# Kernel tuning notes

Measured on AMD Instinct MI355X. Metric: run time of the kernel, lower is better.

The kernel has to match this reference:

```python
import jax, jax.numpy as jnp
import numpy as np

B, C, H, W = 16, 256, 32, 32
N_HEAD, DIM_HEAD = 8, 32  # dim_hidden = 256 == C


def setup_inputs() -> dict:
    key = jax.random.key(0)
    ks = jax.random.split(key, 9)
    s = 1.0 / np.sqrt(C)
    return {
        "x": jax.random.normal(ks[0], (B, C, H, W), dtype=jnp.float32),
        "w_q": jax.random.normal(ks[1], (C, C), dtype=jnp.float32) * s,
        "b_q": jnp.zeros((C,), dtype=jnp.float32),
        "w_k": jax.random.normal(ks[2], (C, C), dtype=jnp.float32) * s,
        "b_k": jnp.zeros((C,), dtype=jnp.float32),
        "w_v": jax.random.normal(ks[3], (C, C), dtype=jnp.float32) * s,
        "b_v": jnp.zeros((C,), dtype=jnp.float32),
        "w_o": jax.random.normal(ks[4], (C, C), dtype=jnp.float32) * s,
        "b_o": jnp.zeros((C,), dtype=jnp.float32),
    }


def reference(x, w_q, b_q, w_k, b_k, w_v, b_v, w_o, b_o):
    b, c, h, w = x.shape
    L = h * w
    scale = DIM_HEAD ** (-0.5)
    xf = x.reshape(b, c, L)  # [b, c, L]

    def proj(wm, bm):
        # 1x1 conv == per-position linear over channels
        y = jnp.einsum('oc,bcl->bol', wm, xf) + bm[None, :, None]
        return y.reshape(b, N_HEAD, DIM_HEAD, L)

    q = proj(w_q, b_q) * scale
    k = proj(w_k, b_k)
    v = proj(w_v, b_v)

    sim = jnp.einsum('bndl,bndm->bnlm', q, k)           # [b, n, L, L]
    att = jax.nn.softmax(sim, axis=-1)
    out = jnp.einsum('bnlm,bndm->bndl', att, v)         # [b, n, d, L]
    out = out.reshape(b, c, L)
    out = jnp.einsum('oc,bcl->bol', w_o, out) + b_o[None, :, None]
    return out.reshape(b, c, h, w)
```

## Files before the change

kernel.cpp:

```cpp
#include <hip/hip_runtime.h>
#include <hip/hip_bf16.h>
#include <math.h>

namespace {
constexpr int B_ = 16, C_ = 256, L_ = 1024, NH_ = 8, DH_ = 32;

typedef __attribute__((ext_vector_type(8))) short short8v;
typedef __attribute__((ext_vector_type(4))) float float4v;

__device__ __forceinline__ short f2bf(float f) {
    unsigned u = __builtin_bit_cast(unsigned, f);
    u += 0x7fffu + ((u >> 16) & 1u);
    return (short)(u >> 16);
}
__device__ __forceinline__ float bf2f(short s) {
    unsigned u = ((unsigned)(unsigned short)s) << 16;
    return __builtin_bit_cast(float, u);
}
__device__ __forceinline__ unsigned pkrn(float a, float b) {
    float2 f; f.x = a; f.y = b;
    __hip_bfloat162 h = __float22bfloat162_rn(f);
    unsigned u;
    __builtin_memcpy(&u, &h, sizeof(u));
    return u;
}
__device__ __forceinline__ void gld16(const short* g, short* l) {
    __builtin_amdgcn_global_load_lds(
        (const __attribute__((address_space(1))) unsigned*)g,
        (__attribute__((address_space(3))) unsigned*)l, 16, 0, 0);
}

__global__ __launch_bounds__(256) void xpose_kernel(
    const float* __restrict__ x, short* __restrict__ xthi)
{
    const int lt = blockIdx.x, ct = blockIdx.y, b = blockIdx.z;
    const int t = threadIdx.x;
    __shared__ float sX[64][68];

#pragma unroll
    for (int e = 0; e < 4; ++e) {
        const int row = e * 16 + (t >> 4);
        const int col = (t & 15) * 4;
        float4 v = *(const float4*)&x[((size_t)b * C_ + ct * 64 + row) * L_ + lt * 64 + col];
        *(float4*)&sX[row][col] = v;
    }
    __syncthreads();

    const int l = t & 63, cg = t >> 6;
    short hi[16];
#pragma unroll
    for (int i = 0; i < 16; ++i) hi[i] = f2bf(sX[cg * 16 + i][l]);
    const size_t base = ((size_t)b * L_ + lt * 64 + l) * C_ + ct * 64 + cg * 16;
    *(short8v*)&xthi[base]     = *(short8v*)&hi[0];
    *(short8v*)&xthi[base + 8] = *(short8v*)&hi[8];
}

__global__ __launch_bounds__(256) void stackw_kernel(
    const float* __restrict__ wq, const float* __restrict__ wk,
    const float* __restrict__ wv, const float* __restrict__ wo,
    short* __restrict__ WA, short* __restrict__ WoA)
{
    const int g = blockIdx.x * 256 + threadIdx.x;
    if (g < 768 * 256) {
        const int o = g >> 8, cc = g & 255;
        const float* src = (o < 256) ? wq : (o < 512) ? wk : wv;
        const float v = src[(size_t)(o & 255) * 256 + cc];
        const short hi = f2bf(v);
        const short lo = f2bf(v - bf2f(hi));
        WA[(size_t)o * 512 + cc]       = hi;
        WA[(size_t)o * 512 + 256 + cc] = lo;
    } else {
        const int g2 = g - 768 * 256;
        const int o = g2 >> 8, cc = g2 & 255;
        const float v = wo[(size_t)o * 256 + cc];
        const short hi = f2bf(v);
        const short lo = f2bf(v - bf2f(hi));
        WoA[(size_t)o * 512 + cc]       = hi;
        WoA[(size_t)o * 512 + 256 + cc] = lo;
    }
}

template <int KTOT, int EPI>
__global__ __launch_bounds__(256, 2) void gemm_kernel(
    const short* __restrict__ A, const short* __restrict__ B0,
    const float* __restrict__ bias0, const float* __restrict__ bias1, const float* __restrict__ bias2,
    float qscale, void* __restrict__ out0, void* __restrict__ out1, void* __restrict__ out2)
{
    const int lt = blockIdx.x, ot = blockIdx.y, b = blockIdx.z;
    const int t = threadIdx.x, wv = t >> 6, lane = t & 63;
    const int quad = lane >> 4, c = lane & 15;
    const int wo = (wv & 1) * 64, wl = (wv >> 1) * 64;

    __shared__ short sA[128 * 32];
    __shared__ short sB[128 * 32];

    float4v acc[4][4];
#pragma unroll
    for (int i = 0; i < 4; ++i)
#pragma unroll
        for (int j = 0; j < 4; ++j) acc[i][j] = (float4v)0.f;

    const short* Arow = A + (size_t)(ot * 128) * KTOT;
    const int srow = t >> 2, sseg = t & 3;

    for (int kk = 0; kk < KTOT / 32; ++kk) {
        const int koff = (kk & 7) * 32;
        __syncthreads();
#pragma unroll
        for (int e = 0; e < 2; ++e) {
            gld16(Arow + (size_t)(e * 64 + srow) * KTOT + kk * 32 + sseg * 8,
                  &sA[(e * 256 + t) * 8]);
            gld16(B0 + ((size_t)b * L_ + lt * 128 + e * 64 + srow) * 256 + koff + sseg * 8,
                  &sB[(e * 256 + t) * 8]);
        }
        __syncthreads();

        short8v af[4], bf[4];
#pragma unroll
        for (int i = 0; i < 4; ++i) af[i] = *(const short8v*)&sA[(wo + 16 * i + c) * 32 + quad * 8];
#pragma unroll
        for (int j = 0; j < 4; ++j) bf[j] = *(const short8v*)&sB[(wl + 16 * j + c) * 32 + quad * 8];
#pragma unroll
        for (int i = 0; i < 4; ++i)
#pragma unroll
            for (int j = 0; j < 4; ++j)
                acc[i][j] = __builtin_amdgcn_mfma_f32_16x16x32_bf16(af[i], bf[j], acc[i][j], 0, 0, 0);
    }

    if constexpr (EPI == 0) {
        const int typ = ot >> 1;
        const int chbase = (ot & 1) * 128 + wo;
        const float* bp = (typ == 0) ? bias0 : (typ == 1) ? bias1 : bias2;
        const float sc = (typ == 0) ? qscale : 1.f;
        short* outp = (short*)((typ == 0) ? out0 : (typ == 1) ? out1 : out2);
        if (typ < 2) {
#pragma unroll
            for (int i = 0; i < 4; ++i) {
                const int ch0 = chbase + 16 * i + quad * 4;
                const int head = ch0 >> 5, d0 = ch0 & 31;
                float bias[4];
#pragma unroll
                for (int r = 0; r < 4; ++r) bias[r] = bp[ch0 + r];
#pragma unroll
                for (int j = 0; j < 4; ++j) {
                    const int l = lt * 128 + wl + 16 * j + c;
                    short4 sv;
                    sv.x = f2bf((acc[i][j][0] + bias[0]) * sc);
                    sv.y = f2bf((acc[i][j][1] + bias[1]) * sc);
                    sv.z = f2bf((acc[i][j][2] + bias[2]) * sc);
                    sv.w = f2bf((acc[i][j][3] + bias[3]) * sc);
                    *(short4*)&outp[(((size_t)b * NH_ + head) * L_ + l) * 32 + d0] = sv;
                }
            }
        } else {
#pragma unroll
            for (int i = 0; i < 4; ++i)
#pragma unroll
                for (int r = 0; r < 4; ++r) {
                    const int ch = chbase + 16 * i + quad * 4 + r;
                    const float bias = bp[ch];
#pragma unroll
                    for (int j = 0; j < 4; ++j)
                        outp[((size_t)b * C_ + ch) * L_ + lt * 128 + wl + 16 * j + c] =
                            f2bf(acc[i][j][r] + bias);
                }
        }
    } else {
        float* outp = (float*)out0;
#pragma unroll
        for (int i = 0; i < 4; ++i)
#pragma unroll
            for (int r = 0; r < 4; ++r) {
                const int ch = ot * 128 + wo + 16 * i + quad * 4 + r;
                const float bias = bias0[ch];
#pragma unroll
                for (int j = 0; j < 4; ++j)
                    outp[((size_t)b * C_ + ch) * L_ + lt * 128 + wl + 16 * j + c] =
                        acc[i][j][r] + bias;
            }
    }
}

__global__ __launch_bounds__(256, 4) void attn_kernel(
    const short* __restrict__ qt,
    const short* __restrict__ kt,
    const short* __restrict__ vb,
    short* __restrict__ athi)
{
    const int flat = blockIdx.x;
    const int g = ((flat >> 6) << 3) | (flat & 7);
    const int chunk = (flat >> 3) & 7;
    const int b = g >> 3, h = g & 7;
    const int t = threadIdx.x;
    const int wv = t >> 6, lane = t & 63;
    const int quad = lane >> 4, c = lane & 15;
    const int lq0 = chunk * 128 + wv * 32;

    __shared__ __align__(16) short sK[2][64 * 32];
    __shared__ __align__(16) short sV[2][2][32 * 32];
    __shared__ __align__(16) short sPT[4][2][16][72];

    const size_t bh = (size_t)b * NH_ + h;
    const short* qbase = qt + (bh * L_) * 32;
    const short* kbase = kt + (bh * L_) * 32;
    const size_t vrow = (size_t)b * C_ + h * DH_;

    short8v qfrag[2];
#pragma unroll
    for (int qf = 0; qf < 2; ++qf)
        qfrag[qf] = *(const short8v*)(qbase + (size_t)(lq0 + qf * 16 + c) * 32 + quad * 8);

    float lp4[2][4];
#pragma unroll
    for (int qf = 0; qf < 2; ++qf)
#pragma unroll
        for (int r = 0; r < 4; ++r) lp4[qf][r] = 0.f;
    float4v o_acc[2][2];
#pragma unroll
    for (int qf = 0; qf < 2; ++qf) { o_acc[qf][0] = (float4v)0.f; o_acc[qf][1] = (float4v)0.f; }

    auto stage = [&](int m0, int buf) {
        gld16(kbase + (size_t)(m0 + (t >> 2)) * 32 + (t & 3) * 8, &sK[buf][t * 8]);
        gld16(vb + (vrow + ((t >> 2) & 31)) * L_ + m0 + (t >> 7) * 32 + (t & 3) * 8,
              (short*)sV[buf] + t * 8);
    };

    stage(0, 0);

    for (int i = 0; i < 16; ++i) {
        __syncthreads();
        if (i < 15) stage((i + 1) * 64, (i + 1) & 1);
        const int buf = i & 1;

        short8v kf[4], vf[2][2];
#pragma unroll
        for (int kb = 0; kb < 4; ++kb)
            kf[kb] = *(const short8v*)&sK[buf][(kb * 16 + c) * 32 + quad * 8];
#pragma unroll
        for (int kc = 0; kc < 2; ++kc)
#pragma unroll
            for (int nb2 = 0; nb2 < 2; ++nb2)
                vf[kc][nb2] = *(const short8v*)&sV[buf][kc][(nb2 * 16 + c) * 32 + quad * 8];

        float4v st[2][4];
#pragma unroll
        for (int qf = 0; qf < 2; ++qf)
#pragma unroll
            for (int kb = 0; kb < 4; ++kb)
                st[qf][kb] = __builtin_amdgcn_mfma_f32_16x16x32_bf16(kf[kb], qfrag[qf], (float4v)0.f, 0, 0, 0);

#pragma unroll
        for (int qf = 0; qf < 2; ++qf)
#pragma unroll
            for (int kb = 0; kb < 4; ++kb) {
                float p[4];
#pragma unroll
                for (int r = 0; r < 4; ++r) {
                    p[r] = __builtin_amdgcn_exp2f(st[qf][kb][r]);
                    lp4[qf][r] += p[r];
                }
                uint2 w;
                w.x = pkrn(p[0], p[1]);
                w.y = pkrn(p[2], p[3]);
                *(uint2*)&sPT[wv][qf][c][kb * 16 + quad * 4] = w;
            }

#pragma unroll
        for (int qf = 0; qf < 2; ++qf)
#pragma unroll
            for (int kc = 0; kc < 2; ++kc) {
                const short8v pf = *(const short8v*)&sPT[wv][qf][c][kc * 32 + quad * 8];
#pragma unroll
                for (int nb2 = 0; nb2 < 2; ++nb2)
                    o_acc[qf][nb2] = __builtin_amdgcn_mfma_f32_16x16x32_bf16(vf[kc][nb2], pf, o_acc[qf][nb2], 0, 0, 0);
            }
    }

#pragma unroll
    for (int qf = 0; qf < 2; ++qf) {
        float l = (lp4[qf][0] + lp4[qf][1]) + (lp4[qf][2] + lp4[qf][3]);
        l += __shfl_xor(l, 16);
        l += __shfl_xor(l, 32);
        const float inv = 1.f / l;
#pragma unroll
        for (int nb2 = 0; nb2 < 2; ++nb2) {
            short4 sv;
            sv.x = f2bf(o_acc[qf][nb2][0] * inv);
            sv.y = f2bf(o_acc[qf][nb2][1] * inv);
            sv.z = f2bf(o_acc[qf][nb2][2] * inv);
            sv.w = f2bf(o_acc[qf][nb2][3] * inv);
            *(short4*)&athi[((size_t)b * L_ + lq0 + qf * 16 + c) * C_ + h * DH_ + nb2 * 16 + quad * 4] = sv;
        }
    }
}

}

extern "C" void kernel_launch(void* const* d_in, const int* in_sizes, int n_in,
                              void* d_out, int out_size, void* d_ws, size_t ws_size,
                              hipStream_t stream) {
    const float* x   = (const float*)d_in[0];
    const float* w_q = (const float*)d_in[1];
    const float* b_q = (const float*)d_in[2];
    const float* w_k = (const float*)d_in[3];
    const float* b_k = (const float*)d_in[4];
    const float* w_v = (const float*)d_in[5];
    const float* b_v = (const float*)d_in[6];
    const float* w_o = (const float*)d_in[7];
    const float* b_o = (const float*)d_in[8];
    float* out = (float*)d_out;

    const size_t NT = (size_t)B_ * L_ * C_;
    short* xthi = (short*)d_ws;
    short* WA   = xthi + NT;
    short* WoA  = WA + 768 * 512;
    short* qt   = WoA + 256 * 512;
    short* kt   = qt + NT;
    short* vb   = kt + NT;
    short* athi = vb + NT;

    const float scale_q = 0.17677669529663687f * 1.4426950408889634f;

    xpose_kernel<<<dim3(L_ / 64, C_ / 64, B_), 256, 0, stream>>>(x, xthi);
    stackw_kernel<<<dim3(1024), 256, 0, stream>>>(w_q, w_k, w_v, w_o, WA, WoA);
    gemm_kernel<512, 0><<<dim3(L_ / 128, 6, B_), 256, 0, stream>>>(
        WA, xthi, b_q, b_k, b_v, scale_q, qt, kt, vb);
    attn_kernel<<<dim3(1024), 256, 0, stream>>>(qt, kt, vb, athi);
    gemm_kernel<512, 1><<<dim3(L_ / 128, 2, B_), 256, 0, stream>>>(
        WoA, athi, b_o, nullptr, nullptr, 1.f, out, nullptr, nullptr);
}
```

Measured before the change: 154.8 us.

## Double K-tile depth in GEMM and attention with XOR-swizzled LDS layouts

```diff
diff --git a/kernel.cpp b/kernel.cpp
--- a/kernel.cpp
+++ b/kernel.cpp
@@ -81,7 +81,7 @@
 }
 
 template <int KTOT, int EPI>
-__global__ __launch_bounds__(256, 2) void gemm_kernel(
+__global__ __launch_bounds__(256, 3) void gemm_kernel(
     const short* __restrict__ A, const short* __restrict__ B0,
     const float* __restrict__ bias0, const float* __restrict__ bias1, const float* __restrict__ bias2,
     float qscale, void* __restrict__ out0, void* __restrict__ out1, void* __restrict__ out2)
@@ -91,8 +91,8 @@
     const int quad = lane >> 4, c = lane & 15;
     const int wo = (wv & 1) * 64, wl = (wv >> 1) * 64;
 
-    __shared__ short sA[128 * 32];
-    __shared__ short sB[128 * 32];
+    __shared__ short sA[128 * 64];
+    __shared__ short sB[128 * 64];
 
     float4v acc[4][4];
 #pragma unroll
@@ -101,30 +101,39 @@
         for (int j = 0; j < 4; ++j) acc[i][j] = (float4v)0.f;
 
     const short* Arow = A + (size_t)(ot * 128) * KTOT;
-    const int srow = t >> 2, sseg = t & 3;
-
-    for (int kk = 0; kk < KTOT / 32; ++kk) {
-        const int koff = (kk & 7) * 32;
+    const int srow = t >> 3, sseg = t & 7;
+    const int seg = sseg ^ (srow & 7);
+
+    for (int kk = 0; kk < KTOT / 64; ++kk) {
         __syncthreads();
 #pragma unroll
-        for (int e = 0; e < 2; ++e) {
-            gld16(Arow + (size_t)(e * 64 + srow) * KTOT + kk * 32 + sseg * 8,
+        for (int e = 0; e < 4; ++e) {
+            gld16(Arow + (size_t)(e * 32 + srow) * KTOT + kk * 64 + seg * 8,
                   &sA[(e * 256 + t) * 8]);
-            gld16(B0 + ((size_t)b * L_ + lt * 128 + e * 64 + srow) * 256 + koff + sseg * 8,
+            gld16(B0 + ((size_t)b * L_ + lt * 128 + e * 32 + srow) * 256 + (kk & 3) * 64 + seg * 8,
                   &sB[(e * 256 + t) * 8]);
         }
         __syncthreads();
 
-        short8v af[4], bf[4];
-#pragma unroll
-        for (int i = 0; i < 4; ++i) af[i] = *(const short8v*)&sA[(wo + 16 * i + c) * 32 + quad * 8];
-#pragma unroll
-        for (int j = 0; j < 4; ++j) bf[j] = *(const short8v*)&sB[(wl + 16 * j + c) * 32 + quad * 8];
-#pragma unroll
-        for (int i = 0; i < 4; ++i)
-#pragma unroll
-            for (int j = 0; j < 4; ++j)
-                acc[i][j] = __builtin_amdgcn_mfma_f32_16x16x32_bf16(af[i], bf[j], acc[i][j], 0, 0, 0);
+#pragma unroll
+        for (int kc2 = 0; kc2 < 2; ++kc2) {
+            short8v af[4], bf[4];
+#pragma unroll
+            for (int i = 0; i < 4; ++i) {
+                const int row = wo + 16 * i + c;
+                af[i] = *(const short8v*)&sA[row * 64 + (((kc2 * 4 + quad) ^ (c & 7)) * 8)];
+            }
+#pragma unroll
+            for (int j = 0; j < 4; ++j) {
+                const int row = wl + 16 * j + c;
+                bf[j] = *(const short8v*)&sB[row * 64 + (((kc2 * 4 + quad) ^ (c & 7)) * 8)];
+            }
+#pragma unroll
+            for (int i = 0; i < 4; ++i)
+#pragma unroll
+                for (int j = 0; j < 4; ++j)
+                    acc[i][j] = __builtin_amdgcn_mfma_f32_16x16x32_bf16(af[i], bf[j], acc[i][j], 0, 0, 0);
+        }
     }
 
     if constexpr (EPI == 0) {
@@ -196,8 +205,8 @@
     const int quad = lane >> 4, c = lane & 15;
     const int lq0 = chunk * 128 + wv * 32;
 
-    __shared__ __align__(16) short sK[2][64 * 32];
-    __shared__ __align__(16) short sV[2][2][32 * 32];
+    __shared__ __align__(16) short sK[2][128 * 32];
+    __shared__ __align__(16) short sV[2][32 * 128];
     __shared__ __align__(16) short sPT[4][2][16][72];
 
     const size_t bh = (size_t)b * NH_ + h;
@@ -220,60 +229,76 @@
     for (int qf = 0; qf < 2; ++qf) { o_acc[qf][0] = (float4v)0.f; o_acc[qf][1] = (float4v)0.f; }
 
     auto stage = [&](int m0, int buf) {
-        gld16(kbase + (size_t)(m0 + (t >> 2)) * 32 + (t & 3) * 8, &sK[buf][t * 8]);
-        gld16(vb + (vrow + ((t >> 2) & 31)) * L_ + m0 + (t >> 7) * 32 + (t & 3) * 8,
-              (short*)sV[buf] + t * 8);
+#pragma unroll
+        for (int e = 0; e < 2; ++e) {
+            const int row = e * 64 + (t >> 2);
+            const int sg = (t & 3) ^ (row & 3);
+            gld16(kbase + (size_t)(m0 + row) * 32 + sg * 8, &sK[buf][(e * 256 + t) * 8]);
+        }
+#pragma unroll
+        for (int e = 0; e < 2; ++e) {
+            const int ch = e * 16 + wv * 4 + (lane >> 4);
+            const int sg = (lane & 15) ^ (ch & 15);
+            gld16(vb + (vrow + ch) * L_ + m0 + sg * 8, &sV[buf][(e * 256 + t) * 8]);
+        }
     };
 
     stage(0, 0);
 
-    for (int i = 0; i < 16; ++i) {
+    for (int i = 0; i < 8; ++i) {
         __syncthreads();
-        if (i < 15) stage((i + 1) * 64, (i + 1) & 1);
+        if (i < 7) stage((i + 1) * 128, (i + 1) & 1);
         const int buf = i & 1;
 
-        short8v kf[4], vf[2][2];
-#pragma unroll
-        for (int kb = 0; kb < 4; ++kb)
-            kf[kb] = *(const short8v*)&sK[buf][(kb * 16 + c) * 32 + quad * 8];
-#pragma unroll
-        for (int kc = 0; kc < 2; ++kc)
-#pragma unroll
-            for (int nb2 = 0; nb2 < 2; ++nb2)
-                vf[kc][nb2] = *(const short8v*)&sV[buf][kc][(nb2 * 16 + c) * 32 + quad * 8];
-
-        float4v st[2][4];
-#pragma unroll
-        for (int qf = 0; qf < 2; ++qf)
-#pragma unroll
-            for (int kb = 0; kb < 4; ++kb)
-                st[qf][kb] = __builtin_amdgcn_mfma_f32_16x16x32_bf16(kf[kb], qfrag[qf], (float4v)0.f, 0, 0, 0);
-
-#pragma unroll
-        for (int qf = 0; qf < 2; ++qf)
+#pragma unroll
+        for (int sub = 0; sub < 2; ++sub) {
+            short8v kf[4], vf[2][2];
 #pragma unroll
             for (int kb = 0; kb < 4; ++kb) {
-                float p[4];
-#pragma unroll
-                for (int r = 0; r < 4; ++r) {
-                    p[r] = __builtin_amdgcn_exp2f(st[qf][kb][r]);
-                    lp4[qf][r] += p[r];
-                }
-                uint2 w;
-                w.x = pkrn(p[0], p[1]);
-                w.y = pkrn(p[2], p[3]);
-                *(uint2*)&sPT[wv][qf][c][kb * 16 + quad * 4] = w;
-            }
-
-#pragma unroll
-        for (int qf = 0; qf < 2; ++qf)
-#pragma unroll
-            for (int kc = 0; kc < 2; ++kc) {
-                const short8v pf = *(const short8v*)&sPT[wv][qf][c][kc * 32 + quad * 8];
-#pragma unroll
-                for (int nb2 = 0; nb2 < 2; ++nb2)
-                    o_acc[qf][nb2] = __builtin_amdgcn_mfma_f32_16x16x32_bf16(vf[kc][nb2], pf, o_acc[qf][nb2], 0, 0, 0);
-            }
+                const int row = sub * 64 + kb * 16 + c;
+                kf[kb] = *(const short8v*)&sK[buf][row * 32 + ((quad ^ (c & 3)) * 8)];
+            }
+#pragma unroll
+            for (int kcL = 0; kcL < 2; ++kcL)
+#pragma unroll
+                for (int nb2 = 0; nb2 < 2; ++nb2) {
+                    const int pos = (sub * 8 + kcL * 4 + quad) ^ c;
+                    vf[kcL][nb2] = *(const short8v*)&sV[buf][(nb2 * 16 + c) * 128 + pos * 8];
+                }
+
+            float4v st[2][4];
+#pragma unroll
+            for (int qf = 0; qf < 2; ++qf)
+#pragma unroll
+                for (int kb = 0; kb < 4; ++kb)
+                    st[qf][kb] = __builtin_amdgcn_mfma_f32_16x16x32_bf16(kf[kb], qfrag[qf], (float4v)0.f, 0, 0, 0);
+
+#pragma unroll
+            for (int qf = 0; qf < 2; ++qf)
+#pragma unroll
+                for (int kb = 0; kb < 4; ++kb) {
+                    float p[4];
+#pragma unroll
+                    for (int r = 0; r < 4; ++r) {
+                        p[r] = __builtin_amdgcn_exp2f(st[qf][kb][r]);
+                        lp4[qf][r] += p[r];
+                    }
+                    uint2 w;
+                    w.x = pkrn(p[0], p[1]);
+                    w.y = pkrn(p[2], p[3]);
+                    *(uint2*)&sPT[wv][qf][c][kb * 16 + quad * 4] = w;
+                }
+
+#pragma unroll
+            for (int qf = 0; qf < 2; ++qf)
+#pragma unroll
+                for (int kcL = 0; kcL < 2; ++kcL) {
+                    const short8v pf = *(const short8v*)&sPT[wv][qf][c][kcL * 32 + quad * 8];
+#pragma unroll
+                    for (int nb2 = 0; nb2 < 2; ++nb2)
+                        o_acc[qf][nb2] = __builtin_amdgcn_mfma_f32_16x16x32_bf16(vf[kcL][nb2], pf, o_acc[qf][nb2], 0, 0, 0);
+                }
+        }
     }
 
 #pragma unroll
```

After: 152.9 us. About the same (-1.2%).
